# Kernel optimization log

Measured on AMD Instinct MI355X. Metric: run time of the kernel, lower is better.

## Reference

```python
import jax, jax.numpy as jnp
import numpy as np

QW, KW = 64, 128          # atom query / key window sizes
PAD = (KW - QW) // 2      # halo on each side of the key window
DEPTH, HEADS = 3, 4

def ln(x):
    m = jnp.mean(x, -1, keepdims=True)
    v = jnp.var(x, -1, keepdims=True)
    return (x - m) * jax.lax.rsqrt(v + 1e-5)

def q_windows(x):
    # x: (B, N, ...) -> (B, n, QW, ...); N assumed multiple of QW
    B, N = x.shape[0], x.shape[1]
    n = N // QW
    return x.reshape((B, n, QW) + x.shape[2:])

def k_windows(x):
    # x: (B, N, ...) -> (B, n, KW, ...) sliding key windows with zero halo padding
    B, N = x.shape[0], x.shape[1]
    n = N // QW
    pad_cfg = [(0, 0), (PAD, n * QW + PAD - N)] + [(0, 0)] * (x.ndim - 2)
    xp = jnp.pad(x, pad_cfg)
    idx = jnp.arange(n)[:, None] * QW + jnp.arange(KW)[None, :]
    return xp[:, idx]


def setup_inputs() -> dict:
    key = jax.random.key(0)
    ks = jax.random.split(key, 24)
    B, N, DS, DP, DT, NT = 2, 8192, 128, 16, 384, 1024
    w = lambda k, shp: (jax.random.normal(k, shp, jnp.float32) / np.sqrt(shp[-2])).astype(jnp.float32)
    inp = {
        'ref_pos': jax.random.normal(ks[0], (B, N, 3), jnp.float32),
        'ref_charge': jax.random.normal(ks[1], (B, N, 1), jnp.float32),
        'ref_mask': jnp.ones((B, N, 1), jnp.float32),
        'ref_element': jax.random.uniform(ks[2], (B, N, 128), jnp.float32),
        'ref_atom_name_chars': jax.random.uniform(ks[3], (B, N, 256), jnp.float32),
        'W_single': w(ks[4], (389, DS)),
        'W_pair': w(ks[5], (5, DP)),
        'W_outer': w(ks[6], (DS, 2 * DP)),
        'Wp_ff1': w(ks[7], (DP, 4 * DP)),
        'Wp_ff2': w(ks[8], (4 * DP, DP)),
        'Wq': w(ks[9], (DEPTH, DS, DS)),
        'Wk': w(ks[10], (DEPTH, DS, DS)),
        'Wv': w(ks[11], (DEPTH, DS, DS)),
        'Wo': w(ks[12], (DEPTH, DS, DS)),
        'Wb': w(ks[13], (DP, HEADS)),
        'Wff1': w(ks[14], (DEPTH, DS, 4 * DS)),
        'Wff2': w(ks[15], (DEPTH, 4 * DS, DS)),
        'W_out': w(ks[16], (DS, DT)),
        'ref_space_uid': jnp.sort(jax.random.randint(ks[17], (B, N), 0, NT), axis=-1),
        'atom_to_token_idx': jnp.sort(jax.random.randint(ks[18], (B, N), 0, NT), axis=-1),
        'n_tokens': NT,
    }
    return inp


def reference(ref_pos, ref_charge, ref_mask, ref_element, ref_atom_name_chars,
              W_single, W_pair, W_outer, Wp_ff1, Wp_ff2,
              Wq, Wk, Wv, Wo, Wb, Wff1, Wff2, W_out,
              ref_space_uid, atom_to_token_idx, n_tokens):
    B, N, _ = ref_pos.shape
    n = N // QW
    feats = jnp.concatenate([ref_pos, ref_charge, ref_mask, ref_element, ref_atom_name_chars], -1)
    s = feats @ W_single                                    # (B,N,DS) atom single repr

    # windowed pairwise geometric features
    pos_i, pos_j = q_windows(ref_pos), k_windows(ref_pos)   # (B,n,QW,3), (B,n,KW,3)
    uid_i, uid_j = q_windows(ref_space_uid), k_windows(ref_space_uid)
    dij = pos_i[:, :, :, None, :] - pos_j[:, :, None, :, :]  # (B,n,QW,KW,3)
    inv = 1.0 / (1.0 + jnp.sum(dij * dij, -1, keepdims=True))
    bij = (uid_i[:, :, :, None] == uid_j[:, :, None, :])
    pf = jnp.concatenate([dij, inv, bij[..., None].astype(dij.dtype)], -1)  # (...,5)
    pair = (pf @ W_pair) * bij[..., None].astype(dij.dtype)  # (B,n,QW,KW,DP)

    # pairwise outer-add from relu(single): Linear(DS->2*DP) split into i/j halves
    p = jax.nn.relu(s) @ W_outer
    DP = pair.shape[-1]
    pi, pj = p[..., :DP], p[..., DP:]
    pair = pair + q_windows(pi)[:, :, :, None, :] + k_windows(pj)[:, :, None, :, :]
    pair = pair + jax.nn.relu(ln(pair) @ Wp_ff1) @ Wp_ff2    # pair FF (residual)
    bias = jnp.einsum('bnqkc,ch->bnhqk', pair, Wb)           # attn pair bias

    # key validity mask for the halo-padded positions
    kidx = jnp.arange(n)[:, None] * QW + jnp.arange(KW)[None, :] - PAD
    kmask = jnp.where((kidx >= 0) & (kidx < N), 0.0, -1e9).astype(s.dtype)  # (n,KW)

    dh = s.shape[-1] // HEADS
    x = s
    for l in range(DEPTH):
        h = ln(x)
        q = q_windows(h @ Wq[l]).reshape(B, n, QW, HEADS, dh)
        k = k_windows(h @ Wk[l]).reshape(B, n, KW, HEADS, dh)
        v = k_windows(h @ Wv[l]).reshape(B, n, KW, HEADS, dh)
        logits = jnp.einsum('bnqhd,bnkhd->bnhqk', q, k) / np.sqrt(dh)
        logits = logits + bias + kmask[None, :, None, None, :]
        a = jax.nn.softmax(logits, -1)
        o = jnp.einsum('bnhqk,bnkhd->bnqhd', a, v).reshape(B, N, -1) @ Wo[l]
        x = x + o
        x = x + jax.nn.relu(ln(x) @ Wff1[l]) @ Wff2[l]

    tok = jax.nn.relu(x @ W_out)                             # (B,N,DT)

    def seg_mean(src, idx_):
        ssum = jax.ops.segment_sum(src, idx_, num_segments=n_tokens)
        cnt = jax.ops.segment_sum(jnp.ones((src.shape[0],), src.dtype), idx_, num_segments=n_tokens)
        return ssum / jnp.clip(cnt, 1.0)[:, None]

    return jax.vmap(seg_mean)(tok, atom_to_token_idx)        # (B, n_tokens, DT)
```

## Files before the change

kernel.cpp:

```cpp
#include <hip/hip_runtime.h>
#include <hip/hip_bf16.h>

#define QW 64
#define KW 128
#define PADW 32
#define DEPTH 3
#define HEADS 4
#define B_ 2
#define N_ 8192
#define DS 128
#define DP 16
#define DT 384
#define NT 1024
#define NWIN (N_ / QW)
#define DH (DS / HEADS)

typedef unsigned short u16;
typedef __attribute__((ext_vector_type(8))) short short8;
typedef __attribute__((ext_vector_type(4))) float f32x4v;
typedef __attribute__((ext_vector_type(4))) unsigned short us4;
typedef __attribute__((ext_vector_type(2))) short s16x2;

__device__ __forceinline__ u16 f2b(float x) {
    union { float f; unsigned u; } v; v.f = x;
    unsigned r = v.u + 0x7fffu + ((v.u >> 16) & 1u);
    return (u16)(r >> 16);
}
__device__ __forceinline__ float b2f(u16 h) {
    union { unsigned u; float f; } v; v.u = ((unsigned)h) << 16; return v.f;
}
__device__ __forceinline__ unsigned f2b2(float a, float b) {
    __hip_bfloat162 h = __float22bfloat162_rn(make_float2(a, b));
    union { __hip_bfloat162 h; unsigned u; } c; c.h = h; return c.u;
}
__device__ __forceinline__ us4 pack4(float a, float b, float c, float d) {
    union { us4 v; unsigned u[2]; } o;
    o.u[0] = f2b2(a, b);
    o.u[1] = f2b2(c, d);
    return o.v;
}
__device__ __forceinline__ us4 pack4_relu(float a, float b, float c, float d) {
    union { us4 v; s16x2 s[2]; unsigned u[2]; } o;
    o.u[0] = f2b2(a, b);
    o.u[1] = f2b2(c, d);
    o.s[0] = __builtin_elementwise_max(o.s[0], (s16x2)0);
    o.s[1] = __builtin_elementwise_max(o.s[1], (s16x2)0);
    return o.v;
}

template <int CTRL>
__device__ __forceinline__ float fdpp(float x) {
    int r = __builtin_amdgcn_update_dpp(0, __builtin_bit_cast(int, x),
                                        CTRL, 0xF, 0xF, true);
    return __builtin_bit_cast(float, r);
}
__device__ __forceinline__ float sum4_dpp(float x) {
    x += fdpp<0xB1>(x);
    x += fdpp<0x4E>(x);
    return x;
}
__device__ __forceinline__ float sum16_dpp(float x) {
    x += fdpp<0xB1>(x);
    x += fdpp<0x4E>(x);
    x += fdpp<0x124>(x);
    x += fdpp<0x128>(x);
    return x;
}
__device__ __forceinline__ float max16_dpp(float x) {
    x = fmaxf(x, fdpp<0xB1>(x));
    x = fmaxf(x, fdpp<0x4E>(x));
    x = fmaxf(x, fdpp<0x124>(x));
    x = fmaxf(x, fdpp<0x128>(x));
    return x;
}

__global__ __launch_bounds__(256) void convw_kernel(
    const float* __restrict__ Wq, const float* __restrict__ Wk,
    const float* __restrict__ Wv, const float* __restrict__ Wo,
    const float* __restrict__ Wff1, const float* __restrict__ Wff2,
    const float* __restrict__ Wout, const float* __restrict__ Wpff1,
    const float* __restrict__ Wpff2, const float* __restrict__ Wb,
    const float* __restrict__ Wsingle, const float* __restrict__ Wouter,
    u16* __restrict__ qkvT, u16* __restrict__ woT, u16* __restrict__ ff1T,
    u16* __restrict__ ff2T, u16* __restrict__ woutT,
    u16* __restrict__ w1T32, u16* __restrict__ wcatT,
    u16* __restrict__ wsT, u16* __restrict__ woutrT)
{
    int idx = blockIdx.x * 256 + threadIdx.x;
    if (idx < 3 * 384 * 128) {
        int l = idx / (384 * 128), r = idx % (384 * 128);
        int n = r / 128, k = r % 128;
        const float* W = (n < 128) ? Wq : (n < 256) ? Wk : Wv;
        qkvT[idx] = f2b(W[(size_t)l * 16384 + k * 128 + (n & 127)]);
    }
    if (idx < 3 * 128 * 128) {
        int l = idx / 16384, r = idx % 16384;
        int n = r / 128, k = r % 128;
        woT[idx] = f2b(Wo[(size_t)l * 16384 + k * 128 + n]);
    }
    if (idx < 3 * 512 * 128) {
        int l = idx / 65536, r = idx % 65536;
        int n = r / 128, k = r % 128;
        ff1T[idx] = f2b(Wff1[(size_t)l * 65536 + k * 512 + n]);
    }
    if (idx < 3 * 128 * 512) {
        int l = idx / 65536, r = idx % 65536;
        int n = r / 512, k = r % 512;
        ff2T[idx] = f2b(Wff2[(size_t)l * 65536 + k * 128 + n]);
    }
    if (idx < 384 * 128) {
        int n = idx / 128, k = idx % 128;
        woutT[idx] = f2b(Wout[(size_t)k * 384 + n]);
    }
    if (idx < 64 * 32) {
        int n = idx >> 5, k = idx & 31;
        w1T32[idx] = (k < 16) ? f2b(Wpff1[k * 64 + n]) : (u16)0;
    }
    if (idx < 16 * 96) {
        int h = idx / 96, k = idx % 96;
        float s = 0.f;
        if (h < 4) {
            if (k < 16) s = Wb[k * 4 + h];
            else if (k < 80) {
                int j = k - 16;
                for (int c = 0; c < 16; ++c) s += Wpff2[j * 16 + c] * Wb[c * 4 + h];
            }
        }
        wcatT[idx] = f2b(s);
    }
    if (idx < 128 * 416) {
        int n = idx / 416, k = idx % 416;
        float v = 0.f;
        if (k < 128)       v = Wsingle[(5 + k) * 128 + n];
        else if (k < 384)  v = Wsingle[(133 + k - 128) * 128 + n];
        else if (k < 387)  v = Wsingle[(k - 384) * 128 + n];
        else if (k == 387) v = Wsingle[3 * 128 + n];
        else if (k == 388) v = Wsingle[4 * 128 + n];
        wsT[idx] = f2b(v);
    }
    if (idx < 32 * 128) {
        int n = idx >> 7, k = idx & 127;
        woutrT[idx] = f2b(Wouter[k * 32 + n]);
    }
}

__global__ __launch_bounds__(256) void embed_gemm(
    const float* __restrict__ pos, const float* __restrict__ charge,
    const float* __restrict__ mask, const float* __restrict__ elem,
    const float* __restrict__ chars, const u16* __restrict__ wsT,
    const u16* __restrict__ woutrT, const u16* __restrict__ qkv0T,
    float* __restrict__ X, float* __restrict__ P, u16* __restrict__ QKVb)
{
    __shared__ __align__(16) u16 As[64 * 424];
    __shared__ float redS[64][4];
    const int LNOFF = 64 * 136;
    int tid = threadIdx.x;
    int row0 = blockIdx.x * 64;

    #pragma unroll
    for (int it = 0; it < 8; ++it) {
        int idx = tid + it * 256;
        int r = idx >> 5, c4 = idx & 31;
        f32x4v v = *(const f32x4v*)(elem + (size_t)(row0 + r) * 128 + c4 * 4);
        *(us4*)&As[r * 424 + c4 * 4] = pack4(v[0], v[1], v[2], v[3]);
    }
    #pragma unroll
    for (int it = 0; it < 16; ++it) {
        int idx = tid + it * 256;
        int r = idx >> 6, c4 = idx & 63;
        f32x4v v = *(const f32x4v*)(chars + (size_t)(row0 + r) * 256 + c4 * 4);
        *(us4*)&As[r * 424 + 128 + c4 * 4] = pack4(v[0], v[1], v[2], v[3]);
    }
    if (tid < 64) {
        int g = row0 + tid;
        As[tid * 424 + 384] = f2b(pos[g * 3]);
        As[tid * 424 + 385] = f2b(pos[g * 3 + 1]);
        As[tid * 424 + 386] = f2b(pos[g * 3 + 2]);
        As[tid * 424 + 387] = f2b(charge[g]);
        As[tid * 424 + 388] = f2b(mask[g]);
        for (int c = 389; c < 416; ++c) As[tid * 424 + c] = 0;
    }
    __syncthreads();

    int wv = tid >> 6, lane = tid & 63, quad = lane >> 4, l16 = lane & 15;
    int wm = (wv & 1) * 32, wn = (wv >> 1) * 64;
    f32x4v acc[2][4];
    #pragma unroll
    for (int i = 0; i < 2; ++i)
        #pragma unroll
        for (int j = 0; j < 4; ++j) acc[i][j] = (f32x4v){0.f, 0.f, 0.f, 0.f};

    #pragma unroll
    for (int kk = 0; kk < 13; ++kk) {
        short8 a0 = *(short8*)&As[(wm + l16) * 424 + kk * 32 + quad * 8];
        short8 a1 = *(short8*)&As[(wm + 16 + l16) * 424 + kk * 32 + quad * 8];
        #pragma unroll
        for (int nt = 0; nt < 4; ++nt) {
            short8 bw = *(const short8*)&wsT[(size_t)(wn + nt * 16 + l16) * 416 +
                                             kk * 32 + quad * 8];
            acc[0][nt] = __builtin_amdgcn_mfma_f32_16x16x32_bf16(a0, bw, acc[0][nt], 0, 0, 0);
            acc[1][nt] = __builtin_amdgcn_mfma_f32_16x16x32_bf16(a1, bw, acc[1][nt], 0, 0, 0);
        }
    }
    __syncthreads();

    #pragma unroll
    for (int mt = 0; mt < 2; ++mt) {
        #pragma unroll
        for (int r = 0; r < 4; ++r) {
            int lrow = wm + mt * 16 + quad * 4 + r;
            int row = row0 + lrow;
            float s = 0.f, ss = 0.f;
            #pragma unroll
            for (int nt = 0; nt < 4; ++nt) {
                float v = acc[mt][nt][r];
                int col = wn + nt * 16 + l16;
                X[(size_t)row * DS + col] = v;
                As[lrow * 136 + col] = f2b(fmaxf(v, 0.f));
                s += v; ss += v * v;
            }
            s  = sum16_dpp(s);
            ss = sum16_dpp(ss);
            if (l16 == 0) {
                redS[lrow][(wv >> 1) * 2]     = s;
                redS[lrow][(wv >> 1) * 2 + 1] = ss;
            }
        }
    }
    __syncthreads();

    #pragma unroll
    for (int mt = 0; mt < 2; ++mt)
        #pragma unroll
        for (int r = 0; r < 4; ++r) {
            int lrow = wm + mt * 16 + quad * 4 + r;
            f32x4v rv = *(f32x4v*)&redS[lrow][0];
            float s = rv[0] + rv[2], ss = rv[1] + rv[3];
            float m = s * (1.f / 128.f);
            float var = ss * (1.f / 128.f) - m * m;
            float rs = __builtin_amdgcn_rsqf(var + 1e-5f);
            #pragma unroll
            for (int nt = 0; nt < 4; ++nt) {
                int col = wn + nt * 16 + l16;
                As[LNOFF + lrow * 136 + col] = f2b((acc[mt][nt][r] - m) * rs);
            }
        }

    {
        f32x4v pacc[2];
        pacc[0] = (f32x4v){0.f, 0.f, 0.f, 0.f};
        pacc[1] = (f32x4v){0.f, 0.f, 0.f, 0.f};
        #pragma unroll
        for (int ks = 0; ks < 4; ++ks) {
            short8 a = *(short8*)&As[(wv * 16 + l16) * 136 + ks * 32 + quad * 8];
            #pragma unroll
            for (int nt = 0; nt < 2; ++nt) {
                short8 bw = *(const short8*)&woutrT[(size_t)(nt * 16 + l16) * 128 +
                                                    ks * 32 + quad * 8];
                pacc[nt] = __builtin_amdgcn_mfma_f32_16x16x32_bf16(a, bw, pacc[nt], 0, 0, 0);
            }
        }
        #pragma unroll
        for (int nt = 0; nt < 2; ++nt)
            #pragma unroll
            for (int r = 0; r < 4; ++r) {
                int row = row0 + wv * 16 + quad * 4 + r;
                P[(size_t)row * 32 + nt * 16 + l16] = pacc[nt][r];
            }
    }
    __syncthreads();

    for (int c = 0; c < 3; ++c) {
        int n0c = c * 128;
        f32x4v qa[2][4];
        #pragma unroll
        for (int i = 0; i < 2; ++i)
            #pragma unroll
            for (int j = 0; j < 4; ++j) qa[i][j] = (f32x4v){0.f, 0.f, 0.f, 0.f};
        #pragma unroll
        for (int ks = 0; ks < 4; ++ks) {
            short8 a0 = *(short8*)&As[LNOFF + (wm + l16) * 136 + ks * 32 + quad * 8];
            short8 a1 = *(short8*)&As[LNOFF + (wm + 16 + l16) * 136 + ks * 32 + quad * 8];
            #pragma unroll
            for (int nt = 0; nt < 4; ++nt) {
                short8 bw = *(const short8*)&qkv0T[(size_t)(n0c + wn + nt * 16 + l16) * 128 +
                                                   ks * 32 + quad * 8];
                qa[0][nt] = __builtin_amdgcn_mfma_f32_16x16x32_bf16(a0, bw, qa[0][nt], 0, 0, 0);
                qa[1][nt] = __builtin_amdgcn_mfma_f32_16x16x32_bf16(a1, bw, qa[1][nt], 0, 0, 0);
            }
        }
        #pragma unroll
        for (int mt = 0; mt < 2; ++mt)
            #pragma unroll
            for (int nt = 0; nt < 4; ++nt)
                #pragma unroll
                for (int r = 0; r < 4; ++r) {
                    int row = row0 + wm + mt * 16 + quad * 4 + r;
                    int col = n0c + wn + nt * 16 + l16;
                    QKVb[(size_t)row * 384 + col] = f2b(qa[mt][nt][r]);
                }
    }
}

__global__ __launch_bounds__(256) void bias_kernel(
    const float* __restrict__ pos, const int* __restrict__ uid,
    const float* __restrict__ P, const float* __restrict__ Wpair,
    const u16* __restrict__ w1T32, const u16* __restrict__ wcatT,
    u16* __restrict__ BIASb)
{
    __shared__ __align__(16) float posjS[128][4];
    __shared__ __align__(16) u16 lpS[4][16 * 24];
    __shared__ __align__(16) u16 A2S[4][16 * 104];

    int tid = threadIdx.x;
    int b  = blockIdx.x >> 11;
    int w  = (blockIdx.x >> 4) & 127;
    int qg = blockIdx.x & 15;

    if (tid < 128) {
        int r = tid;
        int jk = w * QW + r - PADW;
        bool valid = (jk >= 0) && (jk < N_);
        int gk = b * N_ + jk;
        float x = 0.f, y = 0.f, zz = 0.f; int u = 0;
        if (valid) { x = pos[gk * 3]; y = pos[gk * 3 + 1]; zz = pos[gk * 3 + 2]; u = uid[gk]; }
        posjS[r][0] = x; posjS[r][1] = y; posjS[r][2] = zz;
        ((int*)posjS[r])[3] = u;
    }

    int wv = tid >> 6, lane = tid & 63, quad = lane >> 4, l16 = lane & 15;
    int cl = lane >> 2, cg = lane & 3;
    int q = qg * 4 + wv;
    int gq = b * N_ + w * QW + q;

    float xi = pos[gq * 3], yi = pos[gq * 3 + 1], zi = pos[gq * 3 + 2];
    int ui = uid[gq];
    f32x4v pi4 = *(const f32x4v*)(P + (size_t)gq * 32 + cg * 4);
    f32x4v wp[5];
    #pragma unroll
    for (int f = 0; f < 5; ++f)
        wp[f] = *(const f32x4v*)(Wpair + f * 16 + cg * 4);
    short8 w1f[4], wcat[3];
    #pragma unroll
    for (int nt = 0; nt < 4; ++nt)
        w1f[nt] = *(const short8*)&w1T32[(nt * 16 + l16) * 32 + quad * 8];
    #pragma unroll
    for (int ks = 0; ks < 3; ++ks)
        wcat[ks] = *(const short8*)&wcatT[l16 * 96 + ks * 32 + quad * 8];

    f32x4v pjv[8];
    #pragma unroll
    for (int t = 0; t < 8; ++t) {
        int jk = w * QW + t * 16 + cl - PADW;
        bool valid = (jk >= 0) && (jk < N_);
        int gk = b * N_ + jk;
        f32x4v v = (f32x4v){0.f, 0.f, 0.f, 0.f};
        if (valid) v = *(const f32x4v*)(P + (size_t)gk * 32 + 16 + cg * 4);
        pjv[t] = v;
    }

    *(us4*)&A2S[wv][l16 * 104 + 80 + quad * 4] = (us4){0, 0, 0, 0};
    __syncthreads();

    size_t bbase = ((size_t)(b * NWIN + w) * HEADS) * (QW * KW);
    const short8 zero8 = (short8){0, 0, 0, 0, 0, 0, 0, 0};

    #pragma unroll 2
    for (int t = 0; t < 8; ++t) {
        int kk1 = t * 16 + cl;
        f32x4v pj4 = *(const f32x4v*)&posjS[kk1][0];
        float xj = pj4[0], yj = pj4[1], zj = pj4[2];
        int uj = __float_as_int(pj4[3]);
        float dx = xi - xj, dy = yi - yj, dz = zi - zj;
        float inv = __builtin_amdgcn_rcpf(1.f + dx * dx + dy * dy + dz * dz);
        float bf = (ui == uj) ? 1.f : 0.f;
        float pr[4];
        #pragma unroll
        for (int j = 0; j < 4; ++j) {
            float s = fmaf(dx, wp[0][j], fmaf(dy, wp[1][j],
                      fmaf(dz, wp[2][j], fmaf(inv, wp[3][j], wp[4][j]))));
            pr[j] = fmaf(bf, s, pi4[j] + pjv[t][j]);
        }
        float sum = pr[0] + pr[1] + pr[2] + pr[3];
        sum = sum4_dpp(sum);
        float m = sum * (1.f / 16.f);
        float d0 = pr[0] - m, d1 = pr[1] - m, d2 = pr[2] - m, d3 = pr[3] - m;
        float vs = d0 * d0 + d1 * d1 + d2 * d2 + d3 * d3;
        vs = sum4_dpp(vs);
        float rstd = __builtin_amdgcn_rsqf(vs * (1.f / 16.f) + 1e-5f);
        *(us4*)&lpS[wv][cl * 24 + cg * 4] =
            pack4(d0 * rstd, d1 * rstd, d2 * rstd, d3 * rstd);
        *(us4*)&A2S[wv][cl * 104 + cg * 4] = pack4(pr[0], pr[1], pr[2], pr[3]);

        short8 blp = zero8;
        if (quad < 2) blp = *(short8*)&lpS[wv][l16 * 24 + quad * 8];
        #pragma unroll
        for (int nt = 0; nt < 4; ++nt) {
            f32x4v z4 = (f32x4v){0.f, 0.f, 0.f, 0.f};
            z4 = __builtin_amdgcn_mfma_f32_16x16x32_bf16(w1f[nt], blp, z4, 0, 0, 0);
            *(us4*)&A2S[wv][l16 * 104 + 16 + nt * 16 + quad * 4] =
                pack4_relu(z4[0], z4[1], z4[2], z4[3]);
        }
        f32x4v acc = (f32x4v){0.f, 0.f, 0.f, 0.f};
        #pragma unroll
        for (int ks = 0; ks < 3; ++ks) {
            short8 a2 = *(short8*)&A2S[wv][l16 * 104 + ks * 32 + quad * 8];
            acc = __builtin_amdgcn_mfma_f32_16x16x32_bf16(a2, wcat[ks], acc, 0, 0, 0);
        }
        if (l16 < 4) {
            *(us4*)&BIASb[bbase + (size_t)l16 * (QW * KW) + q * KW +
                          t * 16 + quad * 4] = pack4(acc[0], acc[1], acc[2], acc[3]);
        }
    }
}

template <bool LAST>
__global__ __launch_bounds__(256) void wo_ff_fused(
    const u16* __restrict__ Ob, const u16* __restrict__ woT,
    const u16* __restrict__ w1T, const u16* __restrict__ w2T,
    const u16* __restrict__ auxT, float* __restrict__ X,
    u16* __restrict__ OutB)
{
    __shared__ __align__(16) u16 As[16 * 136];
    __shared__ __align__(16) u16 Hs[16 * 520];
    __shared__ __align__(16) float redS[16][8];
    int tid = threadIdx.x;
    int row0 = blockIdx.x * 16;
    int wv = tid >> 6, lane = tid & 63, quad = lane >> 4, l16 = lane & 15;
    int wn = wv * 32;

    {
        int r = tid >> 4, c8 = tid & 15;
        *(short8*)&As[r * 136 + c8 * 8] =
            *(const short8*)&Ob[(size_t)(row0 + r) * 128 + c8 * 8];
    }
    __syncthreads();

    f32x4v acc[2];
    acc[0] = (f32x4v){0.f, 0.f, 0.f, 0.f};
    acc[1] = (f32x4v){0.f, 0.f, 0.f, 0.f};
    #pragma unroll
    for (int ks = 0; ks < 4; ++ks) {
        short8 a = *(short8*)&As[l16 * 136 + ks * 32 + quad * 8];
        #pragma unroll
        for (int nt = 0; nt < 2; ++nt) {
            short8 b = *(const short8*)&woT[(size_t)(wn + nt * 16 + l16) * 128 +
                                            ks * 32 + quad * 8];
            acc[nt] = __builtin_amdgcn_mfma_f32_16x16x32_bf16(a, b, acc[nt], 0, 0, 0);
        }
    }
    __syncthreads();

    #pragma unroll
    for (int r = 0; r < 4; ++r) {
        int lrow = quad * 4 + r;
        int row = row0 + lrow;
        float s = 0.f, ss = 0.f;
        #pragma unroll
        for (int nt = 0; nt < 2; ++nt) {
            int col = wn + nt * 16 + l16;
            float v = acc[nt][r] + X[(size_t)row * DS + col];
            acc[nt][r] = v;
            s += v; ss += v * v;
        }
        s  = sum16_dpp(s);
        ss = sum16_dpp(ss);
        if (l16 == 0) {
            redS[lrow][wv * 2]     = s;
            redS[lrow][wv * 2 + 1] = ss;
        }
    }
    __syncthreads();

    #pragma unroll
    for (int r = 0; r < 4; ++r) {
        int lrow = quad * 4 + r;
        f32x4v rv0 = *(f32x4v*)&redS[lrow][0];
        f32x4v rv1 = *(f32x4v*)&redS[lrow][4];
        float s  = rv0[0] + rv0[2] + rv1[0] + rv1[2];
        float ss = rv0[1] + rv0[3] + rv1[1] + rv1[3];
        float m = s * (1.f / 128.f);
        float var = ss * (1.f / 128.f) - m * m;
        float rs = __builtin_amdgcn_rsqf(var + 1e-5f);
        #pragma unroll
        for (int nt = 0; nt < 2; ++nt) {
            int col = wn + nt * 16 + l16;
            As[lrow * 136 + col] = f2b((acc[nt][r] - m) * rs);
        }
    }
    __syncthreads();

    {
        short8 brow[4];
        #pragma unroll
        for (int ks = 0; ks < 4; ++ks)
            brow[ks] = *(short8*)&As[l16 * 136 + ks * 32 + quad * 8];
        #pragma unroll
        for (int mt = 0; mt < 8; ++mt) {
            int j0 = wv * 128 + mt * 16;
            f32x4v c0 = (f32x4v){0.f, 0.f, 0.f, 0.f};
            #pragma unroll
            for (int ks = 0; ks < 4; ++ks) {
                short8 aw = *(const short8*)&w1T[(size_t)(j0 + l16) * 128 +
                                                 ks * 32 + quad * 8];
                c0 = __builtin_amdgcn_mfma_f32_16x16x32_bf16(aw, brow[ks], c0, 0, 0, 0);
            }
            *(us4*)&Hs[l16 * 520 + j0 + quad * 4] =
                pack4_relu(c0[0], c0[1], c0[2], c0[3]);
        }
    }
    __syncthreads();

    f32x4v acc2[2];
    acc2[0] = (f32x4v){0.f, 0.f, 0.f, 0.f};
    acc2[1] = (f32x4v){0.f, 0.f, 0.f, 0.f};
    #pragma unroll
    for (int ks = 0; ks < 16; ++ks) {
        short8 a = *(short8*)&Hs[l16 * 520 + ks * 32 + quad * 8];
        #pragma unroll
        for (int nt = 0; nt < 2; ++nt) {
            short8 b = *(const short8*)&w2T[(size_t)(wn + nt * 16 + l16) * 512 +
                                            ks * 32 + quad * 8];
            acc2[nt] = __builtin_amdgcn_mfma_f32_16x16x32_bf16(a, b, acc2[nt], 0, 0, 0);
        }
    }

    #pragma unroll
    for (int r = 0; r < 4; ++r) {
        int lrow = quad * 4 + r;
        int row = row0 + lrow;
        float s = 0.f, ss = 0.f;
        #pragma unroll
        for (int nt = 0; nt < 2; ++nt) {
            int col = wn + nt * 16 + l16;
            float v = acc2[nt][r] + acc[nt][r];
            acc2[nt][r] = v;
            X[(size_t)row * DS + col] = v;
            s += v; ss += v * v;
        }
        s  = sum16_dpp(s);
        ss = sum16_dpp(ss);
        if (l16 == 0) {
            redS[lrow][wv * 2]     = s;
            redS[lrow][wv * 2 + 1] = ss;
        }
    }
    __syncthreads();

    #pragma unroll
    for (int r = 0; r < 4; ++r) {
        int lrow = quad * 4 + r;
        float m = 0.f, rs = 1.f;
        if (!LAST) {
            f32x4v rv0 = *(f32x4v*)&redS[lrow][0];
            f32x4v rv1 = *(f32x4v*)&redS[lrow][4];
            float s  = rv0[0] + rv0[2] + rv1[0] + rv1[2];
            float ss = rv0[1] + rv0[3] + rv1[1] + rv1[3];
            m = s * (1.f / 128.f);
            float var = ss * (1.f / 128.f) - m * m;
            rs = __builtin_amdgcn_rsqf(var + 1e-5f);
        }
        #pragma unroll
        for (int nt = 0; nt < 2; ++nt) {
            int col = wn + nt * 16 + l16;
            float v = acc2[nt][r];
            As[lrow * 136 + col] = f2b(LAST ? v : (v - m) * rs);
        }
    }
    __syncthreads();

    {
        short8 arow[4];
        #pragma unroll
        for (int ks = 0; ks < 4; ++ks)
            arow[ks] = *(short8*)&As[l16 * 136 + ks * 32 + quad * 8];
        for (int c = 0; c < 3; ++c) {
            int n0c = c * 128;
            f32x4v qa[2];
            qa[0] = (f32x4v){0.f, 0.f, 0.f, 0.f};
            qa[1] = (f32x4v){0.f, 0.f, 0.f, 0.f};
            #pragma unroll
            for (int ks = 0; ks < 4; ++ks) {
                #pragma unroll
                for (int nt = 0; nt < 2; ++nt) {
                    short8 b = *(const short8*)&auxT[(size_t)(n0c + wn + nt * 16 + l16) * 128 +
                                                     ks * 32 + quad * 8];
                    qa[nt] = __builtin_amdgcn_mfma_f32_16x16x32_bf16(arow[ks], b, qa[nt], 0, 0, 0);
                }
            }
            #pragma unroll
            for (int nt = 0; nt < 2; ++nt)
                #pragma unroll
                for (int r = 0; r < 4; ++r) {
                    int row = row0 + quad * 4 + r;
                    int col = n0c + wn + nt * 16 + l16;
                    float v = qa[nt][r];
                    if (LAST) v = fmaxf(v, 0.f);
                    OutB[(size_t)row * 384 + col] = f2b(v);
                }
        }
    }
}

__global__ __launch_bounds__(256) void attn_kernel(
    const u16* __restrict__ QKV, const u16* __restrict__ BIASb,
    u16* __restrict__ O)
{
    __shared__ __align__(16) u16 sK[128 * 40];
    __shared__ __align__(16) u16 sVt[32 * 152];
    __shared__ __align__(16) u16 sP[64 * 136];

    int tid = threadIdx.x;
    int h = blockIdx.x & 3, w = (blockIdx.x >> 2) & 127, b = blockIdx.x >> 9;
    size_t rowbase = (size_t)b * N_ + w * QW;
    size_t bbase = ((size_t)(b * NWIN + w) * HEADS + h) * (QW * KW);
    const short8 zero8 = (short8){0, 0, 0, 0, 0, 0, 0, 0};
    const bool edge = (w == 0) || (w == NWIN - 1);

    int wv = tid >> 6, lane = tid & 63, quad = lane >> 4, l16 = lane & 15;

    short8 aq = *(const short8*)&QKV[(rowbase + wv * 16 + l16) * 384 + h * DH + quad * 8];

    #pragma unroll
    for (int i = 0; i < 2; ++i) {
        int idx = tid + i * 256;
        int r = idx >> 2, d8 = (idx & 3) * 8;
        int jk = w * QW + r - PADW;
        short8 v = zero8;
        if (jk >= 0 && jk < N_)
            v = *(const short8*)&QKV[((size_t)b * N_ + jk) * 384 + 128 + h * DH + d8];
        *(short8*)&sK[r * 40 + d8] = v;
    }
    {
        int kk = tid >> 1, d0 = (tid & 1) * 16;
        int jk = w * QW + kk - PADW;
        short8 v0 = zero8, v1 = zero8;
        if (jk >= 0 && jk < N_) {
            const u16* src = &QKV[((size_t)b * N_ + jk) * 384 + 256 + h * DH + d0];
            v0 = *(const short8*)src;
            v1 = *(const short8*)(src + 8);
        }
        #pragma unroll
        for (int j = 0; j < 8; ++j) {
            sVt[(d0 + j) * 152 + kk] = (u16)v0[j];
            sVt[(d0 + 8 + j) * 152 + kk] = (u16)v1[j];
        }
    }
    #pragma unroll
    for (int i = 0; i < 4; ++i) {
        int idx = tid + i * 256;
        int q = idx >> 4, c8 = idx & 15;
        *(short8*)&sP[q * 136 + c8 * 8] =
            *(const short8*)&BIASb[bbase + (size_t)q * KW + c8 * 8];
    }
    __syncthreads();

    const float scale = 0.17677669529663687f;

    float e[8][4];
    #pragma unroll
    for (int nt = 0; nt < 8; ++nt) {
        short8 bk = *(short8*)&sK[(nt * 16 + l16) * 40 + quad * 8];
        f32x4v acc = (f32x4v){0.f, 0.f, 0.f, 0.f};
        acc = __builtin_amdgcn_mfma_f32_16x16x32_bf16(aq, bk, acc, 0, 0, 0);
        int kk = nt * 16 + l16;
        float msk = 0.f;
        if (edge) {
            int jk = w * QW + kk - PADW;
            msk = (jk >= 0 && jk < N_) ? 0.f : -1e9f;
        }
        #pragma unroll
        for (int r = 0; r < 4; ++r) {
            int q = wv * 16 + quad * 4 + r;
            e[nt][r] = acc[r] * scale + b2f(sP[q * 136 + kk]) + msk;
        }
    }

    #pragma unroll
    for (int r = 0; r < 4; ++r) {
        float m = e[0][r];
        #pragma unroll
        for (int nt = 1; nt < 8; ++nt) m = fmaxf(m, e[nt][r]);
        m = max16_dpp(m);
        float s = 0.f;
        #pragma unroll
        for (int nt = 0; nt < 8; ++nt) {
            float ev = __expf(e[nt][r] - m);
            e[nt][r] = ev;
            s += ev;
        }
        s = sum16_dpp(s);
        float inv = __builtin_amdgcn_rcpf(s);
        #pragma unroll
        for (int nt = 0; nt < 8; ++nt) e[nt][r] *= inv;
    }

    #pragma unroll
    for (int nt = 0; nt < 8; ++nt) {
        int kk = nt * 16 + l16;
        #pragma unroll
        for (int r = 0; r < 4; ++r) {
            int q = wv * 16 + quad * 4 + r;
            sP[q * 136 + kk] = f2b(e[nt][r]);
        }
    }

    short8 ap[4];
    #pragma unroll
    for (int ks = 0; ks < 4; ++ks)
        ap[ks] = *(short8*)&sP[(wv * 16 + l16) * 136 + ks * 32 + quad * 8];
    #pragma unroll
    for (int nt = 0; nt < 2; ++nt) {
        f32x4v acc = (f32x4v){0.f, 0.f, 0.f, 0.f};
        #pragma unroll
        for (int ks = 0; ks < 4; ++ks) {
            short8 bv = *(short8*)&sVt[(nt * 16 + l16) * 152 + ks * 32 + quad * 8];
            acc = __builtin_amdgcn_mfma_f32_16x16x32_bf16(ap[ks], bv, acc, 0, 0, 0);
        }
        int d = nt * 16 + l16;
        #pragma unroll
        for (int r = 0; r < 4; ++r) {
            int q = wv * 16 + quad * 4 + r;
            O[(rowbase + q) * DS + h * DH + d] = f2b(acc[r]);
        }
    }
}

__global__ __launch_bounds__(128) void seg_kernel(
    const u16* __restrict__ TOKb, const int* __restrict__ idx,
    float* __restrict__ out)
{
    int t = blockIdx.x & (NT - 1);
    int b = blockIdx.x >> 10;
    const int* id = idx + (size_t)b * N_;

    int lo = 0, hi = N_;
    while (lo < hi) { int mid = (lo + hi) >> 1; if (id[mid] < t) lo = mid + 1; else hi = mid; }
    int start = lo;
    hi = N_;
    while (lo < hi) { int mid = (lo + hi) >> 1; if (id[mid] < t + 1) lo = mid + 1; else hi = mid; }
    int end = lo;

    float inv = 1.f / fmaxf((float)(end - start), 1.f);
    if (threadIdx.x < 96) {
        int c4 = threadIdx.x * 4;
        f32x4v s = (f32x4v){0.f, 0.f, 0.f, 0.f};
        for (int r = start; r < end; ++r) {
            us4 v = *(const us4*)&TOKb[((size_t)b * N_ + r) * DT + c4];
            s[0] += b2f(v[0]); s[1] += b2f(v[1]);
            s[2] += b2f(v[2]); s[3] += b2f(v[3]);
        }
        s[0] *= inv; s[1] *= inv; s[2] *= inv; s[3] *= inv;
        *(f32x4v*)&out[((size_t)b * NT + t) * DT + c4] = s;
    }
}

extern "C" void kernel_launch(void* const* d_in, const int* in_sizes, int n_in,
                              void* d_out, int out_size, void* d_ws, size_t ws_size,
                              hipStream_t stream)
{
    const float* ref_pos    = (const float*)d_in[0];
    const float* ref_charge = (const float*)d_in[1];
    const float* ref_mask   = (const float*)d_in[2];
    const float* ref_elem   = (const float*)d_in[3];
    const float* ref_chars  = (const float*)d_in[4];
    const float* W_single   = (const float*)d_in[5];
    const float* W_pair     = (const float*)d_in[6];
    const float* W_outer    = (const float*)d_in[7];
    const float* Wp_ff1     = (const float*)d_in[8];
    const float* Wp_ff2     = (const float*)d_in[9];
    const float* Wq         = (const float*)d_in[10];
    const float* Wk         = (const float*)d_in[11];
    const float* Wv         = (const float*)d_in[12];
    const float* Wo         = (const float*)d_in[13];
    const float* Wb         = (const float*)d_in[14];
    const float* Wff1       = (const float*)d_in[15];
    const float* Wff2       = (const float*)d_in[16];
    const float* W_out      = (const float*)d_in[17];
    const int*   uid        = (const int*)d_in[18];
    const int*   a2t        = (const int*)d_in[19];
    float* out = (float*)d_out;

    const size_t ROWS = (size_t)B_ * N_;
    float* ws = (float*)d_ws;
    float* X    = ws;
    float* P    = X + ROWS * DS;
    u16* QKVb   = (u16*)(P + ROWS * 32);
    u16* Ob     = QKVb + ROWS * 384;
    u16* FFb    = Ob + ROWS * DS;
    u16* BIASb  = FFb + ROWS * 512;
    u16* TOKb   = BIASb + (size_t)B_ * NWIN * HEADS * QW * KW;
    u16* LNb    = TOKb + ROWS * DT;
    u16* qkvT   = LNb + ROWS * DS;
    u16* woT    = qkvT + 3 * 384 * 128;
    u16* ff1T   = woT + 3 * 128 * 128;
    u16* ff2T   = ff1T + 3 * 512 * 128;
    u16* woutT  = ff2T + 3 * 128 * 512;
    u16* w1T32  = woutT + 384 * 128;
    u16* wcatT  = w1T32 + 64 * 32;
    u16* wsT    = wcatT + 16 * 96;
    u16* woutrT = wsT + 128 * 416;

    convw_kernel<<<768, 256, 0, stream>>>(Wq, Wk, Wv, Wo, Wff1, Wff2, W_out,
                                          Wp_ff1, Wp_ff2, Wb, W_single, W_outer,
                                          qkvT, woT, ff1T, ff2T, woutT,
                                          w1T32, wcatT, wsT, woutrT);
    embed_gemm<<<ROWS / 64, 256, 0, stream>>>(ref_pos, ref_charge, ref_mask,
                                              ref_elem, ref_chars, wsT, woutrT,
                                              qkvT, X, P, QKVb);
    bias_kernel<<<4096, 256, 0, stream>>>(ref_pos, uid, P, W_pair,
                                          w1T32, wcatT, BIASb);

    for (int l = 0; l < DEPTH; ++l) {
        attn_kernel<<<B_ * NWIN * HEADS, 256, 0, stream>>>(QKVb, BIASb, Ob);
        if (l < DEPTH - 1) {
            wo_ff_fused<false><<<ROWS / 16, 256, 0, stream>>>(
                Ob, woT + (size_t)l * 128 * 128,
                ff1T + (size_t)l * 512 * 128, ff2T + (size_t)l * 128 * 512,
                qkvT + (size_t)(l + 1) * 384 * 128, X, QKVb);
        } else {
            wo_ff_fused<true><<<ROWS / 16, 256, 0, stream>>>(
                Ob, woT + (size_t)l * 128 * 128,
                ff1T + (size_t)l * 512 * 128, ff2T + (size_t)l * 128 * 512,
                woutT, X, TOKb);
        }
    }

    seg_kernel<<<B_ * NT, 128, 0, stream>>>(TOKb, a2t, out);
}
```

Measured before the change: 369.0 us.

## Make each wave own a full 16-row tile in fused Wo/FF kernel

The fused Wo+FF+next-QKV kernel is restructured so each of the four waves processes its own 16 rows across all 128 output columns. Block-wide syncthreads and the LDS cross-wave LayerNorm reduction go away, along with the final X store when it is the last layer. The grid shrinks by four times. The cost is more accumulator registers per wave, a larger per-wave LDS footprint, and each wave streaming all weights on its own, which may lower occupancy. The attention kernel now stages Q through LDS with a coalesced load instead of reading it straight into per-lane registers.

```diff
diff --git a/kernel.cpp b/kernel.cpp
--- a/kernel.cpp
+++ b/kernel.cpp
@@ -421,74 +421,52 @@
     const u16* __restrict__ auxT, float* __restrict__ X,
     u16* __restrict__ OutB)
 {
-    __shared__ __align__(16) u16 As[16 * 136];
-    __shared__ __align__(16) u16 Hs[16 * 520];
-    __shared__ __align__(16) float redS[16][8];
+    __shared__ __align__(16) u16 AsW[4][16 * 136];
+    __shared__ __align__(16) u16 HsW[4][16 * 520];
     int tid = threadIdx.x;
-    int row0 = blockIdx.x * 16;
     int wv = tid >> 6, lane = tid & 63, quad = lane >> 4, l16 = lane & 15;
-    int wn = wv * 32;
-
-    {
-        int r = tid >> 4, c8 = tid & 15;
-        *(short8*)&As[r * 136 + c8 * 8] =
-            *(const short8*)&Ob[(size_t)(row0 + r) * 128 + c8 * 8];
-    }
-    __syncthreads();
-
-    f32x4v acc[2];
-    acc[0] = (f32x4v){0.f, 0.f, 0.f, 0.f};
-    acc[1] = (f32x4v){0.f, 0.f, 0.f, 0.f};
-    #pragma unroll
-    for (int ks = 0; ks < 4; ++ks) {
-        short8 a = *(short8*)&As[l16 * 136 + ks * 32 + quad * 8];
-        #pragma unroll
-        for (int nt = 0; nt < 2; ++nt) {
-            short8 b = *(const short8*)&woT[(size_t)(wn + nt * 16 + l16) * 128 +
+    int row0 = blockIdx.x * 64 + wv * 16;
+    u16* As = AsW[wv];
+    u16* Hs = HsW[wv];
+
+    short8 af[4];
+    #pragma unroll
+    for (int ks = 0; ks < 4; ++ks)
+        af[ks] = *(const short8*)&Ob[(size_t)(row0 + l16) * 128 + ks * 32 + quad * 8];
+
+    f32x4v acc[8];
+    #pragma unroll
+    for (int nt = 0; nt < 8; ++nt) {
+        f32x4v a = (f32x4v){0.f, 0.f, 0.f, 0.f};
+        #pragma unroll
+        for (int ks = 0; ks < 4; ++ks) {
+            short8 b = *(const short8*)&woT[(size_t)(nt * 16 + l16) * 128 +
                                             ks * 32 + quad * 8];
-            acc[nt] = __builtin_amdgcn_mfma_f32_16x16x32_bf16(a, b, acc[nt], 0, 0, 0);
-        }
-    }
-    __syncthreads();
+            a = __builtin_amdgcn_mfma_f32_16x16x32_bf16(af[ks], b, a, 0, 0, 0);
+        }
+        #pragma unroll
+        for (int r = 0; r < 4; ++r)
+            a[r] += X[(size_t)(row0 + quad * 4 + r) * DS + nt * 16 + l16];
+        acc[nt] = a;
+    }
 
     #pragma unroll
     for (int r = 0; r < 4; ++r) {
-        int lrow = quad * 4 + r;
-        int row = row0 + lrow;
         float s = 0.f, ss = 0.f;
         #pragma unroll
-        for (int nt = 0; nt < 2; ++nt) {
-            int col = wn + nt * 16 + l16;
-            float v = acc[nt][r] + X[(size_t)row * DS + col];
-            acc[nt][r] = v;
+        for (int nt = 0; nt < 8; ++nt) {
+            float v = acc[nt][r];
             s += v; ss += v * v;
         }
         s  = sum16_dpp(s);
         ss = sum16_dpp(ss);
-        if (l16 == 0) {
-            redS[lrow][wv * 2]     = s;
-            redS[lrow][wv * 2 + 1] = ss;
-        }
-    }
-    __syncthreads();
-
-    #pragma unroll
-    for (int r = 0; r < 4; ++r) {
-        int lrow = quad * 4 + r;
-        f32x4v rv0 = *(f32x4v*)&redS[lrow][0];
-        f32x4v rv1 = *(f32x4v*)&redS[lrow][4];
-        float s  = rv0[0] + rv0[2] + rv1[0] + rv1[2];
-        float ss = rv0[1] + rv0[3] + rv1[1] + rv1[3];
         float m = s * (1.f / 128.f);
         float var = ss * (1.f / 128.f) - m * m;
         float rs = __builtin_amdgcn_rsqf(var + 1e-5f);
         #pragma unroll
-        for (int nt = 0; nt < 2; ++nt) {
-            int col = wn + nt * 16 + l16;
-            As[lrow * 136 + col] = f2b((acc[nt][r] - m) * rs);
-        }
-    }
-    __syncthreads();
+        for (int nt = 0; nt < 8; ++nt)
+            As[(quad * 4 + r) * 136 + nt * 16 + l16] = f2b((acc[nt][r] - m) * rs);
+    }
 
     {
         short8 brow[4];
@@ -496,108 +474,84 @@
         for (int ks = 0; ks < 4; ++ks)
             brow[ks] = *(short8*)&As[l16 * 136 + ks * 32 + quad * 8];
         #pragma unroll
-        for (int mt = 0; mt < 8; ++mt) {
-            int j0 = wv * 128 + mt * 16;
+        for (int mt = 0; mt < 32; ++mt) {
             f32x4v c0 = (f32x4v){0.f, 0.f, 0.f, 0.f};
             #pragma unroll
             for (int ks = 0; ks < 4; ++ks) {
-                short8 aw = *(const short8*)&w1T[(size_t)(j0 + l16) * 128 +
+                short8 aw = *(const short8*)&w1T[(size_t)(mt * 16 + l16) * 128 +
                                                  ks * 32 + quad * 8];
                 c0 = __builtin_amdgcn_mfma_f32_16x16x32_bf16(aw, brow[ks], c0, 0, 0, 0);
             }
-            *(us4*)&Hs[l16 * 520 + j0 + quad * 4] =
+            *(us4*)&Hs[l16 * 520 + mt * 16 + quad * 4] =
                 pack4_relu(c0[0], c0[1], c0[2], c0[3]);
         }
     }
-    __syncthreads();
-
-    f32x4v acc2[2];
-    acc2[0] = (f32x4v){0.f, 0.f, 0.f, 0.f};
-    acc2[1] = (f32x4v){0.f, 0.f, 0.f, 0.f};
-    #pragma unroll
-    for (int ks = 0; ks < 16; ++ks) {
-        short8 a = *(short8*)&Hs[l16 * 520 + ks * 32 + quad * 8];
-        #pragma unroll
-        for (int nt = 0; nt < 2; ++nt) {
-            short8 b = *(const short8*)&w2T[(size_t)(wn + nt * 16 + l16) * 512 +
-                                            ks * 32 + quad * 8];
-            acc2[nt] = __builtin_amdgcn_mfma_f32_16x16x32_bf16(a, b, acc2[nt], 0, 0, 0);
-        }
+
+    f32x4v acc2[8];
+    #pragma unroll
+    for (int nt = 0; nt < 8; ++nt) acc2[nt] = (f32x4v){0.f, 0.f, 0.f, 0.f};
+    #pragma unroll
+    for (int kb = 0; kb < 4; ++kb) {
+        short8 hf[4];
+        #pragma unroll
+        for (int ksl = 0; ksl < 4; ++ksl)
+            hf[ksl] = *(short8*)&Hs[l16 * 520 + (kb * 4 + ksl) * 32 + quad * 8];
+        #pragma unroll
+        for (int nt = 0; nt < 8; ++nt)
+            #pragma unroll
+            for (int ksl = 0; ksl < 4; ++ksl) {
+                short8 b = *(const short8*)&w2T[(size_t)(nt * 16 + l16) * 512 +
+                                                (kb * 4 + ksl) * 32 + quad * 8];
+                acc2[nt] = __builtin_amdgcn_mfma_f32_16x16x32_bf16(hf[ksl], b, acc2[nt], 0, 0, 0);
+            }
     }
 
     #pragma unroll
     for (int r = 0; r < 4; ++r) {
-        int lrow = quad * 4 + r;
-        int row = row0 + lrow;
+        float vv[8];
         float s = 0.f, ss = 0.f;
         #pragma unroll
-        for (int nt = 0; nt < 2; ++nt) {
-            int col = wn + nt * 16 + l16;
+        for (int nt = 0; nt < 8; ++nt) {
             float v = acc2[nt][r] + acc[nt][r];
-            acc2[nt][r] = v;
-            X[(size_t)row * DS + col] = v;
+            vv[nt] = v;
+            if (!LAST)
+                X[(size_t)(row0 + quad * 4 + r) * DS + nt * 16 + l16] = v;
             s += v; ss += v * v;
         }
-        s  = sum16_dpp(s);
-        ss = sum16_dpp(ss);
-        if (l16 == 0) {
-            redS[lrow][wv * 2]     = s;
-            redS[lrow][wv * 2 + 1] = ss;
-        }
-    }
-    __syncthreads();
-
-    #pragma unroll
-    for (int r = 0; r < 4; ++r) {
-        int lrow = quad * 4 + r;
         float m = 0.f, rs = 1.f;
         if (!LAST) {
-            f32x4v rv0 = *(f32x4v*)&redS[lrow][0];
-            f32x4v rv1 = *(f32x4v*)&redS[lrow][4];
-            float s  = rv0[0] + rv0[2] + rv1[0] + rv1[2];
-            float ss = rv0[1] + rv0[3] + rv1[1] + rv1[3];
+            s  = sum16_dpp(s);
+            ss = sum16_dpp(ss);
             m = s * (1.f / 128.f);
             float var = ss * (1.f / 128.f) - m * m;
             rs = __builtin_amdgcn_rsqf(var + 1e-5f);
         }
         #pragma unroll
-        for (int nt = 0; nt < 2; ++nt) {
-            int col = wn + nt * 16 + l16;
-            float v = acc2[nt][r];
-            As[lrow * 136 + col] = f2b(LAST ? v : (v - m) * rs);
-        }
-    }
-    __syncthreads();
+        for (int nt = 0; nt < 8; ++nt)
+            As[(quad * 4 + r) * 136 + nt * 16 + l16] =
+                f2b(LAST ? vv[nt] : (vv[nt] - m) * rs);
+    }
 
     {
         short8 arow[4];
         #pragma unroll
         for (int ks = 0; ks < 4; ++ks)
             arow[ks] = *(short8*)&As[l16 * 136 + ks * 32 + quad * 8];
-        for (int c = 0; c < 3; ++c) {
-            int n0c = c * 128;
-            f32x4v qa[2];
-            qa[0] = (f32x4v){0.f, 0.f, 0.f, 0.f};
-            qa[1] = (f32x4v){0.f, 0.f, 0.f, 0.f};
+        #pragma unroll
+        for (int t = 0; t < 24; ++t) {
+            f32x4v qa = (f32x4v){0.f, 0.f, 0.f, 0.f};
             #pragma unroll
             for (int ks = 0; ks < 4; ++ks) {
-                #pragma unroll
-                for (int nt = 0; nt < 2; ++nt) {
-                    short8 b = *(const short8*)&auxT[(size_t)(n0c + wn + nt * 16 + l16) * 128 +
-                                                     ks * 32 + quad * 8];
-                    qa[nt] = __builtin_amdgcn_mfma_f32_16x16x32_bf16(arow[ks], b, qa[nt], 0, 0, 0);
-                }
-            }
-            #pragma unroll
-            for (int nt = 0; nt < 2; ++nt)
-                #pragma unroll
-                for (int r = 0; r < 4; ++r) {
-                    int row = row0 + quad * 4 + r;
-                    int col = n0c + wn + nt * 16 + l16;
-                    float v = qa[nt][r];
-                    if (LAST) v = fmaxf(v, 0.f);
-                    OutB[(size_t)row * 384 + col] = f2b(v);
-                }
+                short8 b = *(const short8*)&auxT[(size_t)(t * 16 + l16) * 128 +
+                                                 ks * 32 + quad * 8];
+                qa = __builtin_amdgcn_mfma_f32_16x16x32_bf16(arow[ks], b, qa, 0, 0, 0);
+            }
+            #pragma unroll
+            for (int r = 0; r < 4; ++r) {
+                float v = qa[r];
+                if (LAST) v = fmaxf(v, 0.f);
+                OutB[(size_t)(row0 + quad * 4 + r) * 384 + t * 16 + l16] = f2b(v);
+            }
         }
     }
 }
@@ -606,6 +560,7 @@
     const u16* __restrict__ QKV, const u16* __restrict__ BIASb,
     u16* __restrict__ O)
 {
+    __shared__ __align__(16) u16 sQ[64 * 40];
     __shared__ __align__(16) u16 sK[128 * 40];
     __shared__ __align__(16) u16 sVt[32 * 152];
     __shared__ __align__(16) u16 sP[64 * 136];
@@ -617,10 +572,11 @@
     const short8 zero8 = (short8){0, 0, 0, 0, 0, 0, 0, 0};
     const bool edge = (w == 0) || (w == NWIN - 1);
 
-    int wv = tid >> 6, lane = tid & 63, quad = lane >> 4, l16 = lane & 15;
-
-    short8 aq = *(const short8*)&QKV[(rowbase + wv * 16 + l16) * 384 + h * DH + quad * 8];
-
+    {
+        int r = tid >> 2, d8 = (tid & 3) * 8;
+        *(short8*)&sQ[r * 40 + d8] =
+            *(const short8*)&QKV[(rowbase + r) * 384 + h * DH + d8];
+    }
     #pragma unroll
     for (int i = 0; i < 2; ++i) {
         int idx = tid + i * 256;
@@ -655,8 +611,10 @@
     }
     __syncthreads();
 
+    int wv = tid >> 6, lane = tid & 63, quad = lane >> 4, l16 = lane & 15;
     const float scale = 0.17677669529663687f;
 
+    short8 aq = *(short8*)&sQ[(wv * 16 + l16) * 40 + quad * 8];
     float e[8][4];
     #pragma unroll
     for (int nt = 0; nt < 8; ++nt) {
@@ -814,12 +772,12 @@
     for (int l = 0; l < DEPTH; ++l) {
         attn_kernel<<<B_ * NWIN * HEADS, 256, 0, stream>>>(QKVb, BIASb, Ob);
         if (l < DEPTH - 1) {
-            wo_ff_fused<false><<<ROWS / 16, 256, 0, stream>>>(
+            wo_ff_fused<false><<<ROWS / 64, 256, 0, stream>>>(
                 Ob, woT + (size_t)l * 128 * 128,
                 ff1T + (size_t)l * 512 * 128, ff2T + (size_t)l * 128 * 512,
                 qkvT + (size_t)(l + 1) * 384 * 128, X, QKVb);
         } else {
-            wo_ff_fused<true><<<ROWS / 16, 256, 0, stream>>>(
+            wo_ff_fused<true><<<ROWS / 64, 256, 0, stream>>>(
                 Ob, woT + (size_t)l * 128 * 128,
                 ff1T + (size_t)l * 512 * 128, ff2T + (size_t)l * 128 * 512,
                 woutT, X, TOKb);
```

New measurement: 473.9 us. 28.4% more time.

## Widen fused Wo/FF kernel to 8 waves and stage Q through LDS

Applied to the files above, without the earlier changes.

The fused Wo+LN+FF+projection kernel now runs 512 threads (8 waves) per 16-row block. Each wave owns 16 output columns instead of 32, so per-wave MFMA chains and register accumulators halve and more waves are available to hide latency. The LayerNorm reductions now combine partials from 8 waves. The final-layer X store is skipped because X is no longer read after the last layer. The attention kernel also loads Q with a coalesced copy into shared memory instead of doing per-wave strided global loads. The cost is more block-level synchronisation and extra LDS per block.

```diff
diff --git a/kernel.cpp b/kernel.cpp
--- a/kernel.cpp
+++ b/kernel.cpp
@@ -415,7 +415,7 @@
 }
 
 template <bool LAST>
-__global__ __launch_bounds__(256) void wo_ff_fused(
+__global__ __launch_bounds__(512) void wo_ff_fused(
     const u16* __restrict__ Ob, const u16* __restrict__ woT,
     const u16* __restrict__ w1T, const u16* __restrict__ w2T,
     const u16* __restrict__ auxT, float* __restrict__ X,
@@ -423,48 +423,34 @@
 {
     __shared__ __align__(16) u16 As[16 * 136];
     __shared__ __align__(16) u16 Hs[16 * 520];
-    __shared__ __align__(16) float redS[16][8];
+    __shared__ __align__(16) float redS[16][16];
     int tid = threadIdx.x;
     int row0 = blockIdx.x * 16;
     int wv = tid >> 6, lane = tid & 63, quad = lane >> 4, l16 = lane & 15;
-    int wn = wv * 32;
-
-    {
+    int wn = wv * 16;
+
+    if (tid < 256) {
         int r = tid >> 4, c8 = tid & 15;
         *(short8*)&As[r * 136 + c8 * 8] =
             *(const short8*)&Ob[(size_t)(row0 + r) * 128 + c8 * 8];
     }
     __syncthreads();
 
-    f32x4v acc[2];
-    acc[0] = (f32x4v){0.f, 0.f, 0.f, 0.f};
-    acc[1] = (f32x4v){0.f, 0.f, 0.f, 0.f};
+    f32x4v acc = (f32x4v){0.f, 0.f, 0.f, 0.f};
     #pragma unroll
     for (int ks = 0; ks < 4; ++ks) {
         short8 a = *(short8*)&As[l16 * 136 + ks * 32 + quad * 8];
-        #pragma unroll
-        for (int nt = 0; nt < 2; ++nt) {
-            short8 b = *(const short8*)&woT[(size_t)(wn + nt * 16 + l16) * 128 +
-                                            ks * 32 + quad * 8];
-            acc[nt] = __builtin_amdgcn_mfma_f32_16x16x32_bf16(a, b, acc[nt], 0, 0, 0);
-        }
-    }
-    __syncthreads();
+        short8 b = *(const short8*)&woT[(size_t)(wn + l16) * 128 + ks * 32 + quad * 8];
+        acc = __builtin_amdgcn_mfma_f32_16x16x32_bf16(a, b, acc, 0, 0, 0);
+    }
 
     #pragma unroll
     for (int r = 0; r < 4; ++r) {
         int lrow = quad * 4 + r;
-        int row = row0 + lrow;
-        float s = 0.f, ss = 0.f;
-        #pragma unroll
-        for (int nt = 0; nt < 2; ++nt) {
-            int col = wn + nt * 16 + l16;
-            float v = acc[nt][r] + X[(size_t)row * DS + col];
-            acc[nt][r] = v;
-            s += v; ss += v * v;
-        }
-        s  = sum16_dpp(s);
-        ss = sum16_dpp(ss);
+        float v = acc[r] + X[(size_t)(row0 + lrow) * DS + wn + l16];
+        acc[r] = v;
+        float s  = sum16_dpp(v);
+        float ss = sum16_dpp(v * v);
         if (l16 == 0) {
             redS[lrow][wv * 2]     = s;
             redS[lrow][wv * 2 + 1] = ss;
@@ -475,18 +461,16 @@
     #pragma unroll
     for (int r = 0; r < 4; ++r) {
         int lrow = quad * 4 + r;
-        f32x4v rv0 = *(f32x4v*)&redS[lrow][0];
-        f32x4v rv1 = *(f32x4v*)&redS[lrow][4];
-        float s  = rv0[0] + rv0[2] + rv1[0] + rv1[2];
-        float ss = rv0[1] + rv0[3] + rv1[1] + rv1[3];
+        f32x4v a0 = *(f32x4v*)&redS[lrow][0];
+        f32x4v a1 = *(f32x4v*)&redS[lrow][4];
+        f32x4v a2 = *(f32x4v*)&redS[lrow][8];
+        f32x4v a3 = *(f32x4v*)&redS[lrow][12];
+        float s  = a0[0] + a0[2] + a1[0] + a1[2] + a2[0] + a2[2] + a3[0] + a3[2];
+        float ss = a0[1] + a0[3] + a1[1] + a1[3] + a2[1] + a2[3] + a3[1] + a3[3];
         float m = s * (1.f / 128.f);
         float var = ss * (1.f / 128.f) - m * m;
         float rs = __builtin_amdgcn_rsqf(var + 1e-5f);
-        #pragma unroll
-        for (int nt = 0; nt < 2; ++nt) {
-            int col = wn + nt * 16 + l16;
-            As[lrow * 136 + col] = f2b((acc[nt][r] - m) * rs);
-        }
+        As[lrow * 136 + wn + l16] = f2b((acc[r] - m) * rs);
     }
     __syncthreads();
 
@@ -496,8 +480,8 @@
         for (int ks = 0; ks < 4; ++ks)
             brow[ks] = *(short8*)&As[l16 * 136 + ks * 32 + quad * 8];
         #pragma unroll
-        for (int mt = 0; mt < 8; ++mt) {
-            int j0 = wv * 128 + mt * 16;
+        for (int mt = 0; mt < 4; ++mt) {
+            int j0 = wv * 64 + mt * 16;
             f32x4v c0 = (f32x4v){0.f, 0.f, 0.f, 0.f};
             #pragma unroll
             for (int ks = 0; ks < 4; ++ks) {
@@ -511,35 +495,23 @@
     }
     __syncthreads();
 
-    f32x4v acc2[2];
-    acc2[0] = (f32x4v){0.f, 0.f, 0.f, 0.f};
-    acc2[1] = (f32x4v){0.f, 0.f, 0.f, 0.f};
+    f32x4v acc2 = (f32x4v){0.f, 0.f, 0.f, 0.f};
     #pragma unroll
     for (int ks = 0; ks < 16; ++ks) {
         short8 a = *(short8*)&Hs[l16 * 520 + ks * 32 + quad * 8];
-        #pragma unroll
-        for (int nt = 0; nt < 2; ++nt) {
-            short8 b = *(const short8*)&w2T[(size_t)(wn + nt * 16 + l16) * 512 +
-                                            ks * 32 + quad * 8];
-            acc2[nt] = __builtin_amdgcn_mfma_f32_16x16x32_bf16(a, b, acc2[nt], 0, 0, 0);
-        }
+        short8 b = *(const short8*)&w2T[(size_t)(wn + l16) * 512 + ks * 32 + quad * 8];
+        acc2 = __builtin_amdgcn_mfma_f32_16x16x32_bf16(a, b, acc2, 0, 0, 0);
     }
 
     #pragma unroll
     for (int r = 0; r < 4; ++r) {
         int lrow = quad * 4 + r;
-        int row = row0 + lrow;
-        float s = 0.f, ss = 0.f;
-        #pragma unroll
-        for (int nt = 0; nt < 2; ++nt) {
-            int col = wn + nt * 16 + l16;
-            float v = acc2[nt][r] + acc[nt][r];
-            acc2[nt][r] = v;
-            X[(size_t)row * DS + col] = v;
-            s += v; ss += v * v;
-        }
-        s  = sum16_dpp(s);
-        ss = sum16_dpp(ss);
+        float v = acc2[r] + acc[r];
+        acc2[r] = v;
+        if (!LAST)
+            X[(size_t)(row0 + lrow) * DS + wn + l16] = v;
+        float s  = sum16_dpp(v);
+        float ss = sum16_dpp(v * v);
         if (l16 == 0) {
             redS[lrow][wv * 2]     = s;
             redS[lrow][wv * 2 + 1] = ss;
@@ -552,20 +524,17 @@
         int lrow = quad * 4 + r;
         float m = 0.f, rs = 1.f;
         if (!LAST) {
-            f32x4v rv0 = *(f32x4v*)&redS[lrow][0];
-            f32x4v rv1 = *(f32x4v*)&redS[lrow][4];
-            float s  = rv0[0] + rv0[2] + rv1[0] + rv1[2];
-            float ss = rv0[1] + rv0[3] + rv1[1] + rv1[3];
+            f32x4v a0 = *(f32x4v*)&redS[lrow][0];
+            f32x4v a1 = *(f32x4v*)&redS[lrow][4];
+            f32x4v a2 = *(f32x4v*)&redS[lrow][8];
+            f32x4v a3 = *(f32x4v*)&redS[lrow][12];
+            float s  = a0[0] + a0[2] + a1[0] + a1[2] + a2[0] + a2[2] + a3[0] + a3[2];
+            float ss = a0[1] + a0[3] + a1[1] + a1[3] + a2[1] + a2[3] + a3[1] + a3[3];
             m = s * (1.f / 128.f);
             float var = ss * (1.f / 128.f) - m * m;
             rs = __builtin_amdgcn_rsqf(var + 1e-5f);
         }
-        #pragma unroll
-        for (int nt = 0; nt < 2; ++nt) {
-            int col = wn + nt * 16 + l16;
-            float v = acc2[nt][r];
-            As[lrow * 136 + col] = f2b(LAST ? v : (v - m) * rs);
-        }
+        As[lrow * 136 + wn + l16] = f2b(LAST ? acc2[r] : (acc2[r] - m) * rs);
     }
     __syncthreads();
 
@@ -574,30 +543,22 @@
         #pragma unroll
         for (int ks = 0; ks < 4; ++ks)
             arow[ks] = *(short8*)&As[l16 * 136 + ks * 32 + quad * 8];
-        for (int c = 0; c < 3; ++c) {
-            int n0c = c * 128;
-            f32x4v qa[2];
-            qa[0] = (f32x4v){0.f, 0.f, 0.f, 0.f};
-            qa[1] = (f32x4v){0.f, 0.f, 0.f, 0.f};
+        #pragma unroll
+        for (int t = 0; t < 3; ++t) {
+            int col0 = wv * 48 + t * 16;
+            f32x4v qa = (f32x4v){0.f, 0.f, 0.f, 0.f};
             #pragma unroll
             for (int ks = 0; ks < 4; ++ks) {
-                #pragma unroll
-                for (int nt = 0; nt < 2; ++nt) {
-                    short8 b = *(const short8*)&auxT[(size_t)(n0c + wn + nt * 16 + l16) * 128 +
-                                                     ks * 32 + quad * 8];
-                    qa[nt] = __builtin_amdgcn_mfma_f32_16x16x32_bf16(arow[ks], b, qa[nt], 0, 0, 0);
-                }
-            }
-            #pragma unroll
-            for (int nt = 0; nt < 2; ++nt)
-                #pragma unroll
-                for (int r = 0; r < 4; ++r) {
-                    int row = row0 + quad * 4 + r;
-                    int col = n0c + wn + nt * 16 + l16;
-                    float v = qa[nt][r];
-                    if (LAST) v = fmaxf(v, 0.f);
-                    OutB[(size_t)row * 384 + col] = f2b(v);
-                }
+                short8 b = *(const short8*)&auxT[(size_t)(col0 + l16) * 128 +
+                                                 ks * 32 + quad * 8];
+                qa = __builtin_amdgcn_mfma_f32_16x16x32_bf16(arow[ks], b, qa, 0, 0, 0);
+            }
+            #pragma unroll
+            for (int r = 0; r < 4; ++r) {
+                float v = qa[r];
+                if (LAST) v = fmaxf(v, 0.f);
+                OutB[(size_t)(row0 + quad * 4 + r) * 384 + col0 + l16] = f2b(v);
+            }
         }
     }
 }
@@ -606,6 +567,7 @@
     const u16* __restrict__ QKV, const u16* __restrict__ BIASb,
     u16* __restrict__ O)
 {
+    __shared__ __align__(16) u16 sQ[64 * 40];
     __shared__ __align__(16) u16 sK[128 * 40];
     __shared__ __align__(16) u16 sVt[32 * 152];
     __shared__ __align__(16) u16 sP[64 * 136];
@@ -617,10 +579,11 @@
     const short8 zero8 = (short8){0, 0, 0, 0, 0, 0, 0, 0};
     const bool edge = (w == 0) || (w == NWIN - 1);
 
-    int wv = tid >> 6, lane = tid & 63, quad = lane >> 4, l16 = lane & 15;
-
-    short8 aq = *(const short8*)&QKV[(rowbase + wv * 16 + l16) * 384 + h * DH + quad * 8];
-
+    {
+        int r = tid >> 2, d8 = (tid & 3) * 8;
+        *(short8*)&sQ[r * 40 + d8] =
+            *(const short8*)&QKV[(rowbase + r) * 384 + h * DH + d8];
+    }
     #pragma unroll
     for (int i = 0; i < 2; ++i) {
         int idx = tid + i * 256;
@@ -655,8 +618,10 @@
     }
     __syncthreads();
 
+    int wv = tid >> 6, lane = tid & 63, quad = lane >> 4, l16 = lane & 15;
     const float scale = 0.17677669529663687f;
 
+    short8 aq = *(short8*)&sQ[(wv * 16 + l16) * 40 + quad * 8];
     float e[8][4];
     #pragma unroll
     for (int nt = 0; nt < 8; ++nt) {
@@ -814,12 +779,12 @@
     for (int l = 0; l < DEPTH; ++l) {
         attn_kernel<<<B_ * NWIN * HEADS, 256, 0, stream>>>(QKVb, BIASb, Ob);
         if (l < DEPTH - 1) {
-            wo_ff_fused<false><<<ROWS / 16, 256, 0, stream>>>(
+            wo_ff_fused<false><<<ROWS / 16, 512, 0, stream>>>(
                 Ob, woT + (size_t)l * 128 * 128,
                 ff1T + (size_t)l * 512 * 128, ff2T + (size_t)l * 128 * 512,
                 qkvT + (size_t)(l + 1) * 384 * 128, X, QKVb);
         } else {
-            wo_ff_fused<true><<<ROWS / 16, 256, 0, stream>>>(
+            wo_ff_fused<true><<<ROWS / 16, 512, 0, stream>>>(
                 Ob, woT + (size_t)l * 128 * 128,
                 ff1T + (size_t)l * 512 * 128, ff2T + (size_t)l * 128 * 512,
                 woutT, X, TOKb);
```

New measurement: 373.7 us. Within noise of the previous version (+1.3%).
